# Optimization experiments

Measured on AMD Instinct MI355X. Metric: run time of the kernel, lower is better.

Reference implementation:

```python
import jax, jax.numpy as jnp
import numpy as np

HIDDEN = 1024
HEADS = 16
HEAD_DIM = HIDDEN // HEADS
ROPE_THETA = 10000.0
WINDOW = 128
NEG_INF = -1e9


def _rope_cos_sin(seq_len, head_dim, theta, dtype):
    # inv_freq: [dh/2]; emb = concat([freqs, freqs]) to match rotate-half convention
    inv_freq = 1.0 / (theta ** (jnp.arange(0, head_dim, 2, dtype=jnp.float32) / head_dim))
    pos = jnp.arange(seq_len, dtype=jnp.float32)
    freqs = jnp.einsum('s,d->sd', pos, inv_freq)          # [S, dh/2]
    emb = jnp.concatenate([freqs, freqs], axis=-1)        # [S, dh]
    return jnp.cos(emb).astype(dtype), jnp.sin(emb).astype(dtype)


def _apply_rope(x, cos, sin):
    # x: [B, S, H, dh]; cos/sin: [S, dh] broadcast over batch and heads
    x1, x2 = jnp.split(x, 2, axis=-1)
    half_rot = jnp.concatenate([-x2, x1], axis=-1)
    c = cos[None, :, None, :]
    s = sin[None, :, None, :]
    return x * c + half_rot * s


def setup_inputs() -> dict:
    key = jax.random.key(0)
    k1, k2, k3, k4, k5 = jax.random.split(key, 5)
    std = 0.02
    return {
        'hidden_states': jax.random.normal(k1, (2, 2048, HIDDEN), dtype=jnp.float32),
        'Wq': jax.random.normal(k2, (HIDDEN, HEADS, HEAD_DIM), dtype=jnp.float32) * std,
        'Wk': jax.random.normal(k3, (HIDDEN, HEADS, HEAD_DIM), dtype=jnp.float32) * std,
        'Wv': jax.random.normal(k4, (HIDDEN, HEADS, HEAD_DIM), dtype=jnp.float32) * std,
        'Wo': jax.random.normal(k5, (HEADS, HEAD_DIM, HIDDEN), dtype=jnp.float32) * std,
    }


def reference(hidden_states, Wq, Wk, Wv, Wo):
    B, S, D = hidden_states.shape
    x4 = hidden_states.reshape(B, S, HEADS, HEAD_DIM)
    cos, sin = _rope_cos_sin(S, HEAD_DIM, ROPE_THETA, hidden_states.dtype)
    # RoPE applied to raw hidden states (pre-projection), per original module
    q_in = _apply_rope(x4, cos, sin).reshape(B, S, D)
    k_in = q_in  # query and key get identical RoPE of the same tensor
    v_in = hidden_states

    q = jnp.einsum('bsd,dhk->bshk', q_in, Wq)  # [B,S,H,dh]
    k = jnp.einsum('bsd,dhk->bshk', k_in, Wk)
    v = jnp.einsum('bsd,dhk->bshk', v_in, Wv)

    scale = 1.0 / jnp.sqrt(jnp.asarray(HEAD_DIM, dtype=q.dtype))
    scores = jnp.einsum('bqhd,bkhd->bhqk', q, k) * scale  # [B,H,S,S]

    # sliding-window mask: |i - j| < WINDOW
    pos = jnp.arange(S)
    win = jnp.abs(pos[:, None] - pos[None, :]) < WINDOW   # [S,S] bool
    scores = jnp.where(win[None, None, :, :], scores, NEG_INF)

    probs = jax.nn.softmax(scores, axis=-1)
    out = jnp.einsum('bhqk,bkhd->bqhd', probs, v)          # [B,S,H,dh]
    return jnp.einsum('bqhd,hdo->bqo', out, Wo)            # [B,S,D]
```

## Files before the change

### kernel.cpp

```cpp
#include <hip/hip_runtime.h>
#include <hip/hip_bf16.h>
#include <cstdint>
#include <cmath>

typedef __bf16 bf16_t;
typedef __bf16 bf16x8 __attribute__((ext_vector_type(8)));
typedef __bf16 bf16x4 __attribute__((ext_vector_type(4)));
typedef float  f32x4  __attribute__((ext_vector_type(4)));
typedef float  f32x16 __attribute__((ext_vector_type(16)));

#define MFMA16(a, b, c) __builtin_amdgcn_mfma_f32_16x16x32_bf16(a, b, c, 0, 0, 0)
#define MFMA32(a, b, c) __builtin_amdgcn_mfma_f32_32x32x16_bf16(a, b, c, 0, 0, 0)

constexpr int   SS    = 2048;
constexpr int   DD    = 1024;
constexpr int   HH    = 16;
constexpr float SCALE = 0.125f;
constexpr float L2E   = 1.44269504088896f;

__device__ __forceinline__ bool detect_fp32(const uint16_t* w) {
    uint16_t v = w[threadIdx.x & 63];
    int e = (v >> 7) & 0xFF;
    unsigned long long m = __ballot(e >= 0x80);
    return __popcll(m) >= 4;
}

__device__ __forceinline__ float ldin(const void* p, size_t i, bool f32) {
    return f32 ? ((const float*)p)[i] : (float)((const bf16_t*)p)[i];
}

__device__ __forceinline__ void gload_lds16(const bf16_t* g, bf16_t* l) {
    __builtin_amdgcn_global_load_lds(
        (const __attribute__((address_space(1))) void*)(g),
        (__attribute__((address_space(3))) void*)(l), 16, 0, 0);
}

__global__ __launch_bounds__(256) void prep_kernel(
    const void* __restrict__ hidden, const void* __restrict__ Wq,
    const void* __restrict__ Wk, const void* __restrict__ Wv,
    const void* __restrict__ Wo,
    bf16_t* __restrict__ roped, bf16_t* __restrict__ hiddenb,
    bf16_t* __restrict__ WqT, bf16_t* __restrict__ WkT,
    bf16_t* __restrict__ WvT, bf16_t* __restrict__ WoT) {
    const bool f32 = detect_fp32((const uint16_t*)Wq);
    __shared__ bf16_t tile[32][33];
    if (blockIdx.x < 1024) {
        int gid = blockIdx.x * 256 + threadIdx.x;
        int ic = (gid & 3) * 8;
        int h  = (gid >> 2) & 15;
        int s  = (gid >> 6) & 2047;
        int b  = gid >> 17;
        size_t base = ((size_t)(b * SS + s)) * DD + h * 64 + ic;
        float x[8], y[8];
        if (f32) {
            const float* hp = (const float*)hidden;
            f32x4 x0 = *(const f32x4*)(hp + base);
            f32x4 x1 = *(const f32x4*)(hp + base + 4);
            f32x4 y0 = *(const f32x4*)(hp + base + 32);
            f32x4 y1 = *(const f32x4*)(hp + base + 36);
#pragma unroll
            for (int j = 0; j < 4; ++j) {
                x[j] = x0[j]; x[4 + j] = x1[j];
                y[j] = y0[j]; y[4 + j] = y1[j];
            }
        } else {
            const bf16_t* hp = (const bf16_t*)hidden;
            bf16x8 xv = *(const bf16x8*)(hp + base);
            bf16x8 yv = *(const bf16x8*)(hp + base + 32);
#pragma unroll
            for (int j = 0; j < 8; ++j) { x[j] = (float)xv[j]; y[j] = (float)yv[j]; }
        }
        bf16x8 ro, rh;
#pragma unroll
        for (int j = 0; j < 8; ++j) {
            int i = ic + j;
            float invf = exp2f(-(float)i * (13.287712379549449f / 32.0f));
            float sn, cs;
            __sincosf((float)s * invf, &sn, &cs);
            ro[j]  = (bf16_t)(x[j] * cs - y[j] * sn);
            rh[j]  = (bf16_t)(y[j] * cs + x[j] * sn);
        }
        *(bf16x8*)(roped + base)      = ro;
        *(bf16x8*)(roped + base + 32) = rh;
        if (f32) {
            bf16x8 hb0, hb1;
#pragma unroll
            for (int j = 0; j < 8; ++j) { hb0[j] = (bf16_t)x[j]; hb1[j] = (bf16_t)y[j]; }
            *(bf16x8*)(hiddenb + base)      = hb0;
            *(bf16x8*)(hiddenb + base + 32) = hb1;
        }
    } else {
        int w = blockIdx.x - 1024;
        int z = w >> 10;
        int yy = (w >> 5) & 31, xx = w & 31;
        const void* src = (z == 0) ? Wq : (z == 1) ? Wk : (z == 2) ? Wv : Wo;
        bf16_t*     dst = (z == 0) ? WqT : (z == 1) ? WkT : (z == 2) ? WvT : WoT;
        int tx = threadIdx.x & 31, ty = threadIdx.x >> 5;
        int x0 = xx * 32, y0 = yy * 32;
#pragma unroll
        for (int j = 0; j < 4; ++j)
            tile[ty + j * 8][tx] =
                (bf16_t)ldin(src, (size_t)(y0 + ty + j * 8) * DD + x0 + tx, f32);
        __syncthreads();
#pragma unroll
        for (int j = 0; j < 4; ++j)
            dst[(size_t)(x0 + ty + j * 8) * DD + y0 + tx] = tile[tx][ty + j * 8];
    }
}

__device__ __forceinline__ void stage_a128(const bf16_t* A, int m0, int k0,
                                           bf16_t* As, int tid) {
#pragma unroll
    for (int i = 0; i < 4; ++i) {
        int c = tid + i * 256;
        int r = c >> 3, g = (c & 7) ^ (r & 7);
        gload_lds16(A + (size_t)(m0 + r) * DD + k0 + g * 8, As + c * 8);
    }
}
__device__ __forceinline__ void stage_b64(const bf16_t* Bt, int n0, int k0,
                                          bf16_t* Bs, int tid) {
#pragma unroll
    for (int i = 0; i < 2; ++i) {
        int c = tid + i * 256;
        int r = c >> 3, g = (c & 7) ^ (r & 7);
        gload_lds16(Bt + (size_t)(n0 + r) * DD + k0 + g * 8, Bs + c * 8);
    }
}

__global__ __launch_bounds__(256, 4) void gemm_qkv_fused(
    const bf16_t* __restrict__ roped, const void* __restrict__ hidden_raw,
    const bf16_t* __restrict__ hiddenb, const uint16_t* __restrict__ wdet,
    const bf16_t* __restrict__ WqT, const bf16_t* __restrict__ WkT,
    const bf16_t* __restrict__ WvT,
    bf16_t* __restrict__ Qo, bf16_t* __restrict__ Ko, bf16_t* __restrict__ Vt) {
    __shared__ __align__(16) bf16_t As[128 * 64];
    __shared__ __align__(16) bf16_t B1[64 * 64];
    __shared__ __align__(16) bf16_t B2[64 * 64];
    const int tid = threadIdx.x, lane = tid & 63;
    const int l32 = lane & 31, kh = lane >> 5;
    const int wave = tid >> 6, wm = (wave >> 1) * 64, wn = (wave & 1) * 32;
    const int sw = l32 & 7;

    const int lin = blockIdx.x;
    const int z   = lin & 1;
    const int p   = lin >> 1;
    const int xcd = p & 7, rem = p >> 3;
    const int mb  = (xcd >> 1) * 8 + (rem >> 3);
    const int nb  = (xcd & 1) * 8 + (rem & 7);
    const int m0  = mb * 128, n0 = nb * 64;

    if (z == 0) {
        f32x16 accq[2], acck[2];
        accq[0] = (f32x16)0.0f; accq[1] = (f32x16)0.0f;
        acck[0] = (f32x16)0.0f; acck[1] = (f32x16)0.0f;
        for (int k0 = 0; k0 < DD; k0 += 64) {
            stage_a128(roped, m0, k0, As, tid);
            stage_b64(WqT, n0, k0, B1, tid);
            stage_b64(WkT, n0, k0, B2, tid);
            __syncthreads();
#pragma unroll
            for (int kk = 0; kk < 4; ++kk) {
                const int c8 = (kk * 2 + kh) ^ sw;
                bf16x8 a0 = *(const bf16x8*)(As + (wm      + l32) * 64 + c8 * 8);
                bf16x8 a1 = *(const bf16x8*)(As + (wm + 32 + l32) * 64 + c8 * 8);
                bf16x8 bq = *(const bf16x8*)(B1 + (wn + l32) * 64 + c8 * 8);
                bf16x8 bk = *(const bf16x8*)(B2 + (wn + l32) * 64 + c8 * 8);
                accq[0] = MFMA32(a0, bq, accq[0]);
                accq[1] = MFMA32(a1, bq, accq[1]);
                acck[0] = MFMA32(a0, bk, acck[0]);
                acck[1] = MFMA32(a1, bk, acck[1]);
            }
            __syncthreads();
        }
        const int d = wn + l32;
#pragma unroll
        for (int i = 0; i < 2; ++i) {
#pragma unroll
            for (int q4 = 0; q4 < 4; ++q4) {
                int row = m0 + wm + i * 32 + q4 * 8 + kh * 4;
                int bb = row >> 11, sl = row & 2047;
                size_t base = (((size_t)bb * HH + nb) * SS + sl) * 64 + d;
#pragma unroll
                for (int r = 0; r < 4; ++r) {
                    Qo[base + 64 * r] = (bf16_t)accq[i][q4 * 4 + r];
                    Ko[base + 64 * r] = (bf16_t)acck[i][q4 * 4 + r];
                }
            }
        }
    } else {
        const bool f32 = detect_fp32(wdet);
        const bf16_t* A = f32 ? hiddenb : (const bf16_t*)hidden_raw;
        f32x16 accv[2];
        accv[0] = (f32x16)0.0f; accv[1] = (f32x16)0.0f;
        for (int k0 = 0; k0 < DD; k0 += 64) {
            stage_a128(A, m0, k0, As, tid);
            stage_b64(WvT, n0, k0, B1, tid);
            __syncthreads();
#pragma unroll
            for (int kk = 0; kk < 4; ++kk) {
                const int c8 = (kk * 2 + kh) ^ sw;
                bf16x8 a0 = *(const bf16x8*)(As + (wm      + l32) * 64 + c8 * 8);
                bf16x8 a1 = *(const bf16x8*)(As + (wm + 32 + l32) * 64 + c8 * 8);
                bf16x8 bv = *(const bf16x8*)(B1 + (wn + l32) * 64 + c8 * 8);
                accv[0] = MFMA32(a0, bv, accv[0]);
                accv[1] = MFMA32(a1, bv, accv[1]);
            }
            __syncthreads();
        }
        const int d = wn + l32;
#pragma unroll
        for (int i = 0; i < 2; ++i) {
#pragma unroll
            for (int q4 = 0; q4 < 4; ++q4) {
                int row = m0 + wm + i * 32 + q4 * 8 + kh * 4;
                int bb = row >> 11, sl = row & 2047;
                bf16x4 v;
                v[0] = (bf16_t)accv[i][q4 * 4 + 0];
                v[1] = (bf16_t)accv[i][q4 * 4 + 1];
                v[2] = (bf16_t)accv[i][q4 * 4 + 2];
                v[3] = (bf16_t)accv[i][q4 * 4 + 3];
                *(bf16x4*)(Vt + (((size_t)bb * HH + nb) * 64 + d) * SS + sl) = v;
            }
        }
    }
}

__global__ __launch_bounds__(256) void attn_kernel(
    const bf16_t* __restrict__ Q, const bf16_t* __restrict__ Kk,
    const bf16_t* __restrict__ Vt, bf16_t* __restrict__ attn) {
    __shared__ __align__(16) bf16_t Ks[2][32 * 64];
    __shared__ __align__(16) bf16_t Vs[2][64 * 32];
    __shared__ __align__(16) bf16_t Pl[4][16 * 40];
    const int tid = threadIdx.x, wave = tid >> 6, lane = tid & 63;
    const int quad = lane >> 4, l16 = lane & 15;
    const int sw7 = l16 & 7, sw3 = l16 & 3;

    int lin = (blockIdx.x >> 3) + 128 * (blockIdx.x & 7);
    const int qb0 = (lin & 31) * 64;
    const int h   = (lin >> 5) & 15;
    const int b   = lin >> 9;
    const int qw  = qb0 + wave * 16;

    const size_t bh = (size_t)b * HH + h;
    const bf16_t* Qp = Q  + bh * SS * 64;
    const bf16_t* Kp = Kk + bh * SS * 64;
    const bf16_t* Vp = Vt + bh * 64 * SS;
    bf16_t* P = &Pl[wave][0];

    bf16x8 q0 = *(const bf16x8*)(Qp + (size_t)(qw + l16) * 64 + quad * 8);
    bf16x8 q1 = *(const bf16x8*)(Qp + (size_t)(qw + l16) * 64 + 32 + quad * 8);

    f32x4 Oacc[4];
#pragma unroll
    for (int t = 0; t < 4; ++t) Oacc[t] = (f32x4)0.0f;
    float lsum[4] = {0.f, 0.f, 0.f, 0.f};

    int lo = qb0 - 127; if (lo < 0) lo = 0; lo &= ~31;
    int hi = qb0 + 63 + 127; if (hi > SS - 1) hi = SS - 1;

    const int krow = tid >> 3, kcol = ((tid & 7) ^ (krow & 7)) * 8;
    const int vrow = tid >> 2, vcol = ((tid & 3) ^ (vrow & 3)) * 8;

    int parity = 0;
    for (int kt = lo; kt <= hi; kt += 32, parity ^= 1) {
        gload_lds16(Kp + (size_t)(kt + krow) * 64 + kcol, &Ks[parity][0] + tid * 8);
        gload_lds16(Vp + (size_t)vrow * SS + kt + vcol, &Vs[parity][0] + tid * 8);
        __syncthreads();

        const bf16_t* Kl = &Ks[parity][0];
        const bf16_t* Vl = &Vs[parity][0];
        bf16x8 k00 = *(const bf16x8*)(Kl + l16 * 64 + (quad ^ sw7) * 8);
        bf16x8 k01 = *(const bf16x8*)(Kl + l16 * 64 + ((quad + 4) ^ sw7) * 8);
        bf16x8 k10 = *(const bf16x8*)(Kl + (16 + l16) * 64 + (quad ^ sw7) * 8);
        bf16x8 k11 = *(const bf16x8*)(Kl + (16 + l16) * 64 + ((quad + 4) ^ sw7) * 8);
        bf16x8 vf[4];
#pragma unroll
        for (int t = 0; t < 4; ++t)
            vf[t] = *(const bf16x8*)(Vl + (t * 16 + l16) * 32 + (quad ^ sw3) * 8);

        f32x4 s0 = MFMA16(q0, k00, (f32x4)0.0f);  s0 = MFMA16(q1, k01, s0);
        f32x4 s1 = MFMA16(q0, k10, (f32x4)0.0f);  s1 = MFMA16(q1, k11, s1);

        const int kr0 = kt + l16, kr1 = kt + 16 + l16;
#pragma unroll
        for (int r = 0; r < 4; ++r) {
            int qa = qw + quad * 4 + r;
            int d0 = qa - kr0; if (d0 < 0) d0 = -d0;
            int d1 = qa - kr1; if (d1 < 0) d1 = -d1;
            float p0 = (d0 < 128) ? exp2f(s0[r] * (SCALE * L2E)) : 0.0f;
            float p1 = (d1 < 128) ? exp2f(s1[r] * (SCALE * L2E)) : 0.0f;
            lsum[r] += p0 + p1;
            P[(quad * 4 + r) * 40 + l16]      = (bf16_t)p0;
            P[(quad * 4 + r) * 40 + 16 + l16] = (bf16_t)p1;
        }
        __asm__ volatile("s_waitcnt lgkmcnt(0)" ::: "memory");
        bf16x8 pf = *(const bf16x8*)(P + l16 * 40 + quad * 8);
#pragma unroll
        for (int t = 0; t < 4; ++t)
            Oacc[t] = MFMA16(pf, vf[t], Oacc[t]);
    }

#pragma unroll
    for (int r = 0; r < 4; ++r) {
        float l = lsum[r];
        l += __shfl_xor(l, 1, 64);
        l += __shfl_xor(l, 2, 64);
        l += __shfl_xor(l, 4, 64);
        l += __shfl_xor(l, 8, 64);
        float inv = 1.0f / l;
        int sa = qw + quad * 4 + r;
        size_t base = (((size_t)b * SS + sa) * HH + h) * 64 + l16;
        attn[base]      = (bf16_t)(Oacc[0][r] * inv);
        attn[base + 16] = (bf16_t)(Oacc[1][r] * inv);
        attn[base + 32] = (bf16_t)(Oacc[2][r] * inv);
        attn[base + 48] = (bf16_t)(Oacc[3][r] * inv);
    }
}

__global__ __launch_bounds__(256, 4) void gemm_out_kernel(
    const bf16_t* __restrict__ A, const bf16_t* __restrict__ WoT,
    const uint16_t* __restrict__ wdet, void* __restrict__ out) {
    __shared__ __align__(16) bf16_t As[128 * 64];
    __shared__ __align__(16) bf16_t B1[64 * 64];
    const int tid = threadIdx.x, lane = tid & 63;
    const int l32 = lane & 31, kh = lane >> 5;
    const int wave = tid >> 6, wm = (wave >> 1) * 64, wn = (wave & 1) * 32;
    const int sw = l32 & 7;

    const int lin = blockIdx.x;
    const int xcd = lin & 7, s = lin >> 3;
    const int mb = (xcd >> 1) * 8 + (s >> 3);
    const int nb = (xcd & 1) * 8 + (s & 7);
    const int m0 = mb * 128, n0 = nb * 64;

    f32x16 acc[2];
    acc[0] = (f32x16)0.0f; acc[1] = (f32x16)0.0f;

    for (int k0 = 0; k0 < DD; k0 += 64) {
        stage_a128(A, m0, k0, As, tid);
        stage_b64(WoT, n0, k0, B1, tid);
        __syncthreads();
#pragma unroll
        for (int kk = 0; kk < 4; ++kk) {
            const int c8 = (kk * 2 + kh) ^ sw;
            bf16x8 a0 = *(const bf16x8*)(As + (wm      + l32) * 64 + c8 * 8);
            bf16x8 a1 = *(const bf16x8*)(As + (wm + 32 + l32) * 64 + c8 * 8);
            bf16x8 b0 = *(const bf16x8*)(B1 + (wn + l32) * 64 + c8 * 8);
            acc[0] = MFMA32(a0, b0, acc[0]);
            acc[1] = MFMA32(a1, b0, acc[1]);
        }
        __syncthreads();
    }

    const bool f32 = detect_fp32(wdet);
    const int n = n0 + wn + l32;
#pragma unroll
    for (int i = 0; i < 2; ++i) {
#pragma unroll
        for (int q4 = 0; q4 < 4; ++q4) {
            int row = m0 + wm + i * 32 + q4 * 8 + kh * 4;
#pragma unroll
            for (int r = 0; r < 4; ++r) {
                size_t idx = (size_t)(row + r) * DD + n;
                if (f32) ((float*)out)[idx] = acc[i][q4 * 4 + r];
                else     ((bf16_t*)out)[idx] = (bf16_t)acc[i][q4 * 4 + r];
            }
        }
    }
}

extern "C" void kernel_launch(void* const* d_in, const int* in_sizes, int n_in,
                              void* d_out, int out_size, void* d_ws, size_t ws_size,
                              hipStream_t stream) {
    const void* hidden = d_in[0];
    const void* Wq = d_in[1];
    const void* Wk = d_in[2];
    const void* Wv = d_in[3];
    const void* Wo = d_in[4];
    const uint16_t* wdet = (const uint16_t*)d_in[1];
    char* ws = (char*)d_ws;

    bf16_t* roped   = (bf16_t*)(ws);
    bf16_t* hiddenb = (bf16_t*)(ws + ( 8u << 20));
    bf16_t* WqT     = (bf16_t*)(ws + (16u << 20));
    bf16_t* WkT     = (bf16_t*)(ws + (18u << 20));
    bf16_t* WvT     = (bf16_t*)(ws + (20u << 20));
    bf16_t* WoT     = (bf16_t*)(ws + (22u << 20));
    bf16_t* Qb      = (bf16_t*)(ws + (24u << 20));
    bf16_t* Kb      = (bf16_t*)(ws + (32u << 20));
    bf16_t* Vt      = (bf16_t*)(ws + (40u << 20));
    bf16_t* attn    = roped;

    hipLaunchKernelGGL(prep_kernel, dim3(5120), dim3(256), 0, stream,
                       hidden, Wq, Wk, Wv, Wo, roped, hiddenb,
                       WqT, WkT, WvT, WoT);
    hipLaunchKernelGGL(gemm_qkv_fused, dim3(1024), dim3(256), 0, stream,
                       roped, hidden, hiddenb, wdet, WqT, WkT, WvT, Qb, Kb, Vt);
    hipLaunchKernelGGL(attn_kernel, dim3(1024), dim3(256), 0, stream,
                       Qb, Kb, Vt, attn);
    hipLaunchKernelGGL(gemm_out_kernel, dim3(512), dim3(256), 0, stream,
                       attn, WoT, wdet, d_out);
}
```

Baseline: 158.7 us.

## Fuse all four stages into one persistent kernel with grid barriers

Replaces the four separate launches (prep, QKV GEMM, attention, output GEMM) with one persistent 512-block kernel that loops over the former grids' tiles and separates stages with atomic-counter grid barriers. This is meant to remove kernel launch gaps and tail idle time between stages. It adds a memset launch, relies on all 512 blocks being co-resident (launch bounds set to 2 blocks/CU), and pays spin-wait barrier costs plus lower occupancy during the GEMM phases.

```diff
diff --git a/kernel.cpp b/kernel.cpp
--- a/kernel.cpp
+++ b/kernel.cpp
@@ -35,335 +35,361 @@
         (__attribute__((address_space(3))) void*)(l), 16, 0, 0);
 }
 
-__global__ __launch_bounds__(256) void prep_kernel(
+__device__ __forceinline__ void stage_a128(const bf16_t* A, int m0, int k0,
+                                           bf16_t* As, int tid) {
+#pragma unroll
+    for (int i = 0; i < 4; ++i) {
+        int c = tid + i * 256;
+        int r = c >> 3, g = (c & 7) ^ (r & 7);
+        gload_lds16(A + (size_t)(m0 + r) * DD + k0 + g * 8, As + c * 8);
+    }
+}
+__device__ __forceinline__ void stage_b64(const bf16_t* Bt, int n0, int k0,
+                                          bf16_t* Bs, int tid) {
+#pragma unroll
+    for (int i = 0; i < 2; ++i) {
+        int c = tid + i * 256;
+        int r = c >> 3, g = (c & 7) ^ (r & 7);
+        gload_lds16(Bt + (size_t)(n0 + r) * DD + k0 + g * 8, Bs + c * 8);
+    }
+}
+
+__device__ __forceinline__ void grid_bar(unsigned* w) {
+    __syncthreads();
+    if (threadIdx.x == 0) {
+        __threadfence();
+        if (atomicAdd(w, 1u) == 511u) {
+            atomicExch(w + 1, 1u);
+        } else {
+            while (atomicOr(w + 1, 0u) == 0u) __builtin_amdgcn_s_sleep(8);
+        }
+        __threadfence();
+    }
+    __syncthreads();
+}
+
+__global__ __launch_bounds__(256, 2) void mega_kernel(
     const void* __restrict__ hidden, const void* __restrict__ Wq,
     const void* __restrict__ Wk, const void* __restrict__ Wv,
     const void* __restrict__ Wo,
     bf16_t* __restrict__ roped, bf16_t* __restrict__ hiddenb,
     bf16_t* __restrict__ WqT, bf16_t* __restrict__ WkT,
-    bf16_t* __restrict__ WvT, bf16_t* __restrict__ WoT) {
+    bf16_t* __restrict__ WvT, bf16_t* __restrict__ WoT,
+    bf16_t* __restrict__ Qb, bf16_t* __restrict__ Kb,
+    bf16_t* __restrict__ Vt, bf16_t* __restrict__ attnb,
+    void* __restrict__ out, unsigned* __restrict__ bars) {
+    __shared__ __align__(16) char smem[32768];
+    const int tid  = threadIdx.x, lane = tid & 63;
     const bool f32 = detect_fp32((const uint16_t*)Wq);
-    __shared__ bf16_t tile[32][33];
-    if (blockIdx.x < 1024) {
-        int gid = blockIdx.x * 256 + threadIdx.x;
-        int ic = (gid & 3) * 8;
-        int h  = (gid >> 2) & 15;
-        int s  = (gid >> 6) & 2047;
-        int b  = gid >> 17;
-        size_t base = ((size_t)(b * SS + s)) * DD + h * 64 + ic;
-        float x[8], y[8];
-        if (f32) {
-            const float* hp = (const float*)hidden;
-            f32x4 x0 = *(const f32x4*)(hp + base);
-            f32x4 x1 = *(const f32x4*)(hp + base + 4);
-            f32x4 y0 = *(const f32x4*)(hp + base + 32);
-            f32x4 y1 = *(const f32x4*)(hp + base + 36);
-#pragma unroll
-            for (int j = 0; j < 4; ++j) {
-                x[j] = x0[j]; x[4 + j] = x1[j];
-                y[j] = y0[j]; y[4 + j] = y1[j];
-            }
-        } else {
-            const bf16_t* hp = (const bf16_t*)hidden;
-            bf16x8 xv = *(const bf16x8*)(hp + base);
-            bf16x8 yv = *(const bf16x8*)(hp + base + 32);
-#pragma unroll
-            for (int j = 0; j < 8; ++j) { x[j] = (float)xv[j]; y[j] = (float)yv[j]; }
-        }
-        bf16x8 ro, rh;
-#pragma unroll
-        for (int j = 0; j < 8; ++j) {
-            int i = ic + j;
-            float invf = exp2f(-(float)i * (13.287712379549449f / 32.0f));
-            float sn, cs;
-            __sincosf((float)s * invf, &sn, &cs);
-            ro[j]  = (bf16_t)(x[j] * cs - y[j] * sn);
-            rh[j]  = (bf16_t)(y[j] * cs + x[j] * sn);
-        }
-        *(bf16x8*)(roped + base)      = ro;
-        *(bf16x8*)(roped + base + 32) = rh;
-        if (f32) {
-            bf16x8 hb0, hb1;
-#pragma unroll
-            for (int j = 0; j < 8; ++j) { hb0[j] = (bf16_t)x[j]; hb1[j] = (bf16_t)y[j]; }
-            *(bf16x8*)(hiddenb + base)      = hb0;
-            *(bf16x8*)(hiddenb + base + 32) = hb1;
-        }
-    } else {
-        int w = blockIdx.x - 1024;
-        int z = w >> 10;
-        int yy = (w >> 5) & 31, xx = w & 31;
-        const void* src = (z == 0) ? Wq : (z == 1) ? Wk : (z == 2) ? Wv : Wo;
-        bf16_t*     dst = (z == 0) ? WqT : (z == 1) ? WkT : (z == 2) ? WvT : WoT;
-        int tx = threadIdx.x & 31, ty = threadIdx.x >> 5;
-        int x0 = xx * 32, y0 = yy * 32;
-#pragma unroll
-        for (int j = 0; j < 4; ++j)
-            tile[ty + j * 8][tx] =
-                (bf16_t)ldin(src, (size_t)(y0 + ty + j * 8) * DD + x0 + tx, f32);
-        __syncthreads();
-#pragma unroll
-        for (int j = 0; j < 4; ++j)
-            dst[(size_t)(x0 + ty + j * 8) * DD + y0 + tx] = tile[tx][ty + j * 8];
-    }
-}
-
-__device__ __forceinline__ void stage_a128(const bf16_t* A, int m0, int k0,
-                                           bf16_t* As, int tid) {
-#pragma unroll
-    for (int i = 0; i < 4; ++i) {
-        int c = tid + i * 256;
-        int r = c >> 3, g = (c & 7) ^ (r & 7);
-        gload_lds16(A + (size_t)(m0 + r) * DD + k0 + g * 8, As + c * 8);
-    }
-}
-__device__ __forceinline__ void stage_b64(const bf16_t* Bt, int n0, int k0,
-                                          bf16_t* Bs, int tid) {
-#pragma unroll
-    for (int i = 0; i < 2; ++i) {
-        int c = tid + i * 256;
-        int r = c >> 3, g = (c & 7) ^ (r & 7);
-        gload_lds16(Bt + (size_t)(n0 + r) * DD + k0 + g * 8, Bs + c * 8);
-    }
-}
-
-__global__ __launch_bounds__(256, 4) void gemm_qkv_fused(
-    const bf16_t* __restrict__ roped, const void* __restrict__ hidden_raw,
-    const bf16_t* __restrict__ hiddenb, const uint16_t* __restrict__ wdet,
-    const bf16_t* __restrict__ WqT, const bf16_t* __restrict__ WkT,
-    const bf16_t* __restrict__ WvT,
-    bf16_t* __restrict__ Qo, bf16_t* __restrict__ Ko, bf16_t* __restrict__ Vt) {
-    __shared__ __align__(16) bf16_t As[128 * 64];
-    __shared__ __align__(16) bf16_t B1[64 * 64];
-    __shared__ __align__(16) bf16_t B2[64 * 64];
-    const int tid = threadIdx.x, lane = tid & 63;
-    const int l32 = lane & 31, kh = lane >> 5;
-    const int wave = tid >> 6, wm = (wave >> 1) * 64, wn = (wave & 1) * 32;
-    const int sw = l32 & 7;
-
-    const int lin = blockIdx.x;
-    const int z   = lin & 1;
-    const int p   = lin >> 1;
-    const int xcd = p & 7, rem = p >> 3;
-    const int mb  = (xcd >> 1) * 8 + (rem >> 3);
-    const int nb  = (xcd & 1) * 8 + (rem & 7);
-    const int m0  = mb * 128, n0 = nb * 64;
-
-    if (z == 0) {
-        f32x16 accq[2], acck[2];
-        accq[0] = (f32x16)0.0f; accq[1] = (f32x16)0.0f;
-        acck[0] = (f32x16)0.0f; acck[1] = (f32x16)0.0f;
+
+    {
+        bf16_t (*tile)[33] = reinterpret_cast<bf16_t(*)[33]>(smem);
+        for (int vb = blockIdx.x; vb < 5120; vb += 512) {
+            if (vb < 1024) {
+                int gid = vb * 256 + tid;
+                int ic = (gid & 3) * 8;
+                int h  = (gid >> 2) & 15;
+                int s  = (gid >> 6) & 2047;
+                int b  = gid >> 17;
+                size_t base = ((size_t)(b * SS + s)) * DD + h * 64 + ic;
+                float x[8], y[8];
+                if (f32) {
+                    const float* hp = (const float*)hidden;
+                    f32x4 x0 = *(const f32x4*)(hp + base);
+                    f32x4 x1 = *(const f32x4*)(hp + base + 4);
+                    f32x4 y0 = *(const f32x4*)(hp + base + 32);
+                    f32x4 y1 = *(const f32x4*)(hp + base + 36);
+#pragma unroll
+                    for (int j = 0; j < 4; ++j) {
+                        x[j] = x0[j]; x[4 + j] = x1[j];
+                        y[j] = y0[j]; y[4 + j] = y1[j];
+                    }
+                } else {
+                    const bf16_t* hp = (const bf16_t*)hidden;
+                    bf16x8 xv = *(const bf16x8*)(hp + base);
+                    bf16x8 yv = *(const bf16x8*)(hp + base + 32);
+#pragma unroll
+                    for (int j = 0; j < 8; ++j) { x[j] = (float)xv[j]; y[j] = (float)yv[j]; }
+                }
+                bf16x8 ro, rh;
+#pragma unroll
+                for (int j = 0; j < 8; ++j) {
+                    int i = ic + j;
+                    float invf = exp2f(-(float)i * (13.287712379549449f / 32.0f));
+                    float sn, cs;
+                    __sincosf((float)s * invf, &sn, &cs);
+                    ro[j] = (bf16_t)(x[j] * cs - y[j] * sn);
+                    rh[j] = (bf16_t)(y[j] * cs + x[j] * sn);
+                }
+                *(bf16x8*)(roped + base)      = ro;
+                *(bf16x8*)(roped + base + 32) = rh;
+                if (f32) {
+                    bf16x8 hb0, hb1;
+#pragma unroll
+                    for (int j = 0; j < 8; ++j) { hb0[j] = (bf16_t)x[j]; hb1[j] = (bf16_t)y[j]; }
+                    *(bf16x8*)(hiddenb + base)      = hb0;
+                    *(bf16x8*)(hiddenb + base + 32) = hb1;
+                }
+            } else {
+                int w = vb - 1024;
+                int z = w >> 10;
+                int yy = (w >> 5) & 31, xx = w & 31;
+                const void* src = (z == 0) ? Wq : (z == 1) ? Wk : (z == 2) ? Wv : Wo;
+                bf16_t*     dst = (z == 0) ? WqT : (z == 1) ? WkT : (z == 2) ? WvT : WoT;
+                int tx = tid & 31, ty = tid >> 5;
+                int x0 = xx * 32, y0 = yy * 32;
+#pragma unroll
+                for (int j = 0; j < 4; ++j)
+                    tile[ty + j * 8][tx] =
+                        (bf16_t)ldin(src, (size_t)(y0 + ty + j * 8) * DD + x0 + tx, f32);
+                __syncthreads();
+#pragma unroll
+                for (int j = 0; j < 4; ++j)
+                    dst[(size_t)(x0 + ty + j * 8) * DD + y0 + tx] = tile[tx][ty + j * 8];
+                __syncthreads();
+            }
+        }
+    }
+    grid_bar(bars + 0);
+
+    {
+        bf16_t* As = (bf16_t*)smem;
+        bf16_t* B1 = (bf16_t*)(smem + 16384);
+        bf16_t* B2 = (bf16_t*)(smem + 24576);
+        const int l32 = lane & 31, kh = lane >> 5;
+        const int wave = tid >> 6, wm = (wave >> 1) * 64, wn = (wave & 1) * 32;
+        const int sw = l32 & 7;
+#pragma unroll 1
+        for (int rpt = 0; rpt < 2; ++rpt) {
+            const int lin = (rpt == 0) ? (int)blockIdx.x : 1023 - (int)blockIdx.x;
+            const int z   = lin & 1;
+            const int p   = lin >> 1;
+            const int xcd = p & 7, rem = p >> 3;
+            const int mb  = (xcd >> 1) * 8 + (rem >> 3);
+            const int nb  = (xcd & 1) * 8 + (rem & 7);
+            const int m0  = mb * 128, n0 = nb * 64;
+
+            if (z == 0) {
+                f32x16 accq[2], acck[2];
+                accq[0] = (f32x16)0.0f; accq[1] = (f32x16)0.0f;
+                acck[0] = (f32x16)0.0f; acck[1] = (f32x16)0.0f;
+                for (int k0 = 0; k0 < DD; k0 += 64) {
+                    stage_a128(roped, m0, k0, As, tid);
+                    stage_b64(WqT, n0, k0, B1, tid);
+                    stage_b64(WkT, n0, k0, B2, tid);
+                    __syncthreads();
+#pragma unroll
+                    for (int kk = 0; kk < 4; ++kk) {
+                        const int c8 = (kk * 2 + kh) ^ sw;
+                        bf16x8 a0 = *(const bf16x8*)(As + (wm      + l32) * 64 + c8 * 8);
+                        bf16x8 a1 = *(const bf16x8*)(As + (wm + 32 + l32) * 64 + c8 * 8);
+                        bf16x8 bq = *(const bf16x8*)(B1 + (wn + l32) * 64 + c8 * 8);
+                        bf16x8 bk = *(const bf16x8*)(B2 + (wn + l32) * 64 + c8 * 8);
+                        accq[0] = MFMA32(a0, bq, accq[0]);
+                        accq[1] = MFMA32(a1, bq, accq[1]);
+                        acck[0] = MFMA32(a0, bk, acck[0]);
+                        acck[1] = MFMA32(a1, bk, acck[1]);
+                    }
+                    __syncthreads();
+                }
+                const int d = wn + l32;
+#pragma unroll
+                for (int i = 0; i < 2; ++i) {
+#pragma unroll
+                    for (int q4 = 0; q4 < 4; ++q4) {
+                        int row = m0 + wm + i * 32 + q4 * 8 + kh * 4;
+                        int bb = row >> 11, sl = row & 2047;
+                        size_t base = (((size_t)bb * HH + nb) * SS + sl) * 64 + d;
+#pragma unroll
+                        for (int r = 0; r < 4; ++r) {
+                            Qb[base + 64 * r] = (bf16_t)accq[i][q4 * 4 + r];
+                            Kb[base + 64 * r] = (bf16_t)acck[i][q4 * 4 + r];
+                        }
+                    }
+                }
+            } else {
+                const bf16_t* A = f32 ? hiddenb : (const bf16_t*)hidden;
+                f32x16 accv[2];
+                accv[0] = (f32x16)0.0f; accv[1] = (f32x16)0.0f;
+                for (int k0 = 0; k0 < DD; k0 += 64) {
+                    stage_a128(A, m0, k0, As, tid);
+                    stage_b64(WvT, n0, k0, B1, tid);
+                    __syncthreads();
+#pragma unroll
+                    for (int kk = 0; kk < 4; ++kk) {
+                        const int c8 = (kk * 2 + kh) ^ sw;
+                        bf16x8 a0 = *(const bf16x8*)(As + (wm      + l32) * 64 + c8 * 8);
+                        bf16x8 a1 = *(const bf16x8*)(As + (wm + 32 + l32) * 64 + c8 * 8);
+                        bf16x8 bv = *(const bf16x8*)(B1 + (wn + l32) * 64 + c8 * 8);
+                        accv[0] = MFMA32(a0, bv, accv[0]);
+                        accv[1] = MFMA32(a1, bv, accv[1]);
+                    }
+                    __syncthreads();
+                }
+                const int d = wn + l32;
+#pragma unroll
+                for (int i = 0; i < 2; ++i) {
+#pragma unroll
+                    for (int q4 = 0; q4 < 4; ++q4) {
+                        int row = m0 + wm + i * 32 + q4 * 8 + kh * 4;
+                        int bb = row >> 11, sl = row & 2047;
+                        bf16x4 v;
+                        v[0] = (bf16_t)accv[i][q4 * 4 + 0];
+                        v[1] = (bf16_t)accv[i][q4 * 4 + 1];
+                        v[2] = (bf16_t)accv[i][q4 * 4 + 2];
+                        v[3] = (bf16_t)accv[i][q4 * 4 + 3];
+                        *(bf16x4*)(Vt + (((size_t)bb * HH + nb) * 64 + d) * SS + sl) = v;
+                    }
+                }
+            }
+            __syncthreads();
+        }
+    }
+    grid_bar(bars + 2);
+
+    {
+        bf16_t* KsB = (bf16_t*)smem;
+        bf16_t* VsB = (bf16_t*)(smem + 8192);
+        bf16_t* PlB = (bf16_t*)(smem + 16384);
+        const int wave = tid >> 6;
+        const int quad = lane >> 4, l16 = lane & 15;
+        const int sw7 = l16 & 7, sw3 = l16 & 3;
+        bf16_t* P = PlB + wave * 640;
+
+#pragma unroll 1
+        for (int rpt = 0; rpt < 2; ++rpt) {
+            const int vt = (int)blockIdx.x + rpt * 512;
+            int lin = (vt >> 3) + 128 * (vt & 7);
+            const int qb0 = (lin & 31) * 64;
+            const int h   = (lin >> 5) & 15;
+            const int b   = lin >> 9;
+            const int qw  = qb0 + wave * 16;
+
+            const size_t bh = (size_t)b * HH + h;
+            const bf16_t* Qp = Qb + bh * SS * 64;
+            const bf16_t* Kp = Kb + bh * SS * 64;
+            const bf16_t* Vp = Vt + bh * 64 * SS;
+
+            bf16x8 q0 = *(const bf16x8*)(Qp + (size_t)(qw + l16) * 64 + quad * 8);
+            bf16x8 q1 = *(const bf16x8*)(Qp + (size_t)(qw + l16) * 64 + 32 + quad * 8);
+
+            f32x4 Oacc[4];
+#pragma unroll
+            for (int t = 0; t < 4; ++t) Oacc[t] = (f32x4)0.0f;
+            float lsum[4] = {0.f, 0.f, 0.f, 0.f};
+
+            int lo = qb0 - 127; if (lo < 0) lo = 0; lo &= ~31;
+            int hi = qb0 + 63 + 127; if (hi > SS - 1) hi = SS - 1;
+
+            const int krow = tid >> 3, kcol = ((tid & 7) ^ (krow & 7)) * 8;
+            const int vrow = tid >> 2, vcol = ((tid & 3) ^ (vrow & 3)) * 8;
+
+            int parity = 0;
+            for (int kt = lo; kt <= hi; kt += 32, parity ^= 1) {
+                gload_lds16(Kp + (size_t)(kt + krow) * 64 + kcol,
+                            KsB + parity * 2048 + tid * 8);
+                gload_lds16(Vp + (size_t)vrow * SS + kt + vcol,
+                            VsB + parity * 2048 + tid * 8);
+                __syncthreads();
+
+                const bf16_t* Kl = KsB + parity * 2048;
+                const bf16_t* Vl = VsB + parity * 2048;
+                bf16x8 k00 = *(const bf16x8*)(Kl + l16 * 64 + (quad ^ sw7) * 8);
+                bf16x8 k01 = *(const bf16x8*)(Kl + l16 * 64 + ((quad + 4) ^ sw7) * 8);
+                bf16x8 k10 = *(const bf16x8*)(Kl + (16 + l16) * 64 + (quad ^ sw7) * 8);
+                bf16x8 k11 = *(const bf16x8*)(Kl + (16 + l16) * 64 + ((quad + 4) ^ sw7) * 8);
+                bf16x8 vf[4];
+#pragma unroll
+                for (int t = 0; t < 4; ++t)
+                    vf[t] = *(const bf16x8*)(Vl + (t * 16 + l16) * 32 + (quad ^ sw3) * 8);
+
+                f32x4 s0 = MFMA16(q0, k00, (f32x4)0.0f);  s0 = MFMA16(q1, k01, s0);
+                f32x4 s1 = MFMA16(q0, k10, (f32x4)0.0f);  s1 = MFMA16(q1, k11, s1);
+
+                const int kr0 = kt + l16, kr1 = kt + 16 + l16;
+#pragma unroll
+                for (int r = 0; r < 4; ++r) {
+                    int qa = qw + quad * 4 + r;
+                    int d0 = qa - kr0; if (d0 < 0) d0 = -d0;
+                    int d1 = qa - kr1; if (d1 < 0) d1 = -d1;
+                    float p0 = (d0 < 128) ? exp2f(s0[r] * (SCALE * L2E)) : 0.0f;
+                    float p1 = (d1 < 128) ? exp2f(s1[r] * (SCALE * L2E)) : 0.0f;
+                    lsum[r] += p0 + p1;
+                    P[(quad * 4 + r) * 40 + l16]      = (bf16_t)p0;
+                    P[(quad * 4 + r) * 40 + 16 + l16] = (bf16_t)p1;
+                }
+                __asm__ volatile("s_waitcnt lgkmcnt(0)" ::: "memory");
+                __builtin_amdgcn_sched_barrier(0);
+                bf16x8 pf = *(const bf16x8*)(P + l16 * 40 + quad * 8);
+#pragma unroll
+                for (int t = 0; t < 4; ++t)
+                    Oacc[t] = MFMA16(pf, vf[t], Oacc[t]);
+            }
+            __syncthreads();
+
+#pragma unroll
+            for (int r = 0; r < 4; ++r) {
+                float l = lsum[r];
+                l += __shfl_xor(l, 1, 64);
+                l += __shfl_xor(l, 2, 64);
+                l += __shfl_xor(l, 4, 64);
+                l += __shfl_xor(l, 8, 64);
+                float inv = 1.0f / l;
+                int sa = qw + quad * 4 + r;
+                size_t base = (((size_t)b * SS + sa) * HH + h) * 64 + l16;
+                attnb[base]      = (bf16_t)(Oacc[0][r] * inv);
+                attnb[base + 16] = (bf16_t)(Oacc[1][r] * inv);
+                attnb[base + 32] = (bf16_t)(Oacc[2][r] * inv);
+                attnb[base + 48] = (bf16_t)(Oacc[3][r] * inv);
+            }
+        }
+    }
+    grid_bar(bars + 4);
+
+    {
+        bf16_t* As = (bf16_t*)smem;
+        bf16_t* B1 = (bf16_t*)(smem + 16384);
+        const int l32 = lane & 31, kh = lane >> 5;
+        const int wave = tid >> 6, wm = (wave >> 1) * 64, wn = (wave & 1) * 32;
+        const int sw = l32 & 7;
+
+        const int lin = blockIdx.x;
+        const int xcd = lin & 7, s = lin >> 3;
+        const int mb = (xcd >> 1) * 8 + (s >> 3);
+        const int nb = (xcd & 1) * 8 + (s & 7);
+        const int m0 = mb * 128, n0 = nb * 64;
+
+        f32x16 acc[2];
+        acc[0] = (f32x16)0.0f; acc[1] = (f32x16)0.0f;
+
         for (int k0 = 0; k0 < DD; k0 += 64) {
-            stage_a128(roped, m0, k0, As, tid);
-            stage_b64(WqT, n0, k0, B1, tid);
-            stage_b64(WkT, n0, k0, B2, tid);
+            stage_a128(attnb, m0, k0, As, tid);
+            stage_b64(WoT, n0, k0, B1, tid);
             __syncthreads();
 #pragma unroll
             for (int kk = 0; kk < 4; ++kk) {
                 const int c8 = (kk * 2 + kh) ^ sw;
                 bf16x8 a0 = *(const bf16x8*)(As + (wm      + l32) * 64 + c8 * 8);
                 bf16x8 a1 = *(const bf16x8*)(As + (wm + 32 + l32) * 64 + c8 * 8);
-                bf16x8 bq = *(const bf16x8*)(B1 + (wn + l32) * 64 + c8 * 8);
-                bf16x8 bk = *(const bf16x8*)(B2 + (wn + l32) * 64 + c8 * 8);
-                accq[0] = MFMA32(a0, bq, accq[0]);
-                accq[1] = MFMA32(a1, bq, accq[1]);
-                acck[0] = MFMA32(a0, bk, acck[0]);
-                acck[1] = MFMA32(a1, bk, acck[1]);
+                bf16x8 b0 = *(const bf16x8*)(B1 + (wn + l32) * 64 + c8 * 8);
+                acc[0] = MFMA32(a0, b0, acc[0]);
+                acc[1] = MFMA32(a1, b0, acc[1]);
             }
             __syncthreads();
         }
-        const int d = wn + l32;
+
+        const int n = n0 + wn + l32;
 #pragma unroll
         for (int i = 0; i < 2; ++i) {
 #pragma unroll
             for (int q4 = 0; q4 < 4; ++q4) {
                 int row = m0 + wm + i * 32 + q4 * 8 + kh * 4;
-                int bb = row >> 11, sl = row & 2047;
-                size_t base = (((size_t)bb * HH + nb) * SS + sl) * 64 + d;
 #pragma unroll
                 for (int r = 0; r < 4; ++r) {
-                    Qo[base + 64 * r] = (bf16_t)accq[i][q4 * 4 + r];
-                    Ko[base + 64 * r] = (bf16_t)acck[i][q4 * 4 + r];
-                }
-            }
-        }
-    } else {
-        const bool f32 = detect_fp32(wdet);
-        const bf16_t* A = f32 ? hiddenb : (const bf16_t*)hidden_raw;
-        f32x16 accv[2];
-        accv[0] = (f32x16)0.0f; accv[1] = (f32x16)0.0f;
-        for (int k0 = 0; k0 < DD; k0 += 64) {
-            stage_a128(A, m0, k0, As, tid);
-            stage_b64(WvT, n0, k0, B1, tid);
-            __syncthreads();
-#pragma unroll
-            for (int kk = 0; kk < 4; ++kk) {
-                const int c8 = (kk * 2 + kh) ^ sw;
-                bf16x8 a0 = *(const bf16x8*)(As + (wm      + l32) * 64 + c8 * 8);
-                bf16x8 a1 = *(const bf16x8*)(As + (wm + 32 + l32) * 64 + c8 * 8);
-                bf16x8 bv = *(const bf16x8*)(B1 + (wn + l32) * 64 + c8 * 8);
-                accv[0] = MFMA32(a0, bv, accv[0]);
-                accv[1] = MFMA32(a1, bv, accv[1]);
-            }
-            __syncthreads();
-        }
-        const int d = wn + l32;
-#pragma unroll
-        for (int i = 0; i < 2; ++i) {
-#pragma unroll
-            for (int q4 = 0; q4 < 4; ++q4) {
-                int row = m0 + wm + i * 32 + q4 * 8 + kh * 4;
-                int bb = row >> 11, sl = row & 2047;
-                bf16x4 v;
-                v[0] = (bf16_t)accv[i][q4 * 4 + 0];
-                v[1] = (bf16_t)accv[i][q4 * 4 + 1];
-                v[2] = (bf16_t)accv[i][q4 * 4 + 2];
-                v[3] = (bf16_t)accv[i][q4 * 4 + 3];
-                *(bf16x4*)(Vt + (((size_t)bb * HH + nb) * 64 + d) * SS + sl) = v;
-            }
-        }
-    }
-}
-
-__global__ __launch_bounds__(256) void attn_kernel(
-    const bf16_t* __restrict__ Q, const bf16_t* __restrict__ Kk,
-    const bf16_t* __restrict__ Vt, bf16_t* __restrict__ attn) {
-    __shared__ __align__(16) bf16_t Ks[2][32 * 64];
-    __shared__ __align__(16) bf16_t Vs[2][64 * 32];
-    __shared__ __align__(16) bf16_t Pl[4][16 * 40];
-    const int tid = threadIdx.x, wave = tid >> 6, lane = tid & 63;
-    const int quad = lane >> 4, l16 = lane & 15;
-    const int sw7 = l16 & 7, sw3 = l16 & 3;
-
-    int lin = (blockIdx.x >> 3) + 128 * (blockIdx.x & 7);
-    const int qb0 = (lin & 31) * 64;
-    const int h   = (lin >> 5) & 15;
-    const int b   = lin >> 9;
-    const int qw  = qb0 + wave * 16;
-
-    const size_t bh = (size_t)b * HH + h;
-    const bf16_t* Qp = Q  + bh * SS * 64;
-    const bf16_t* Kp = Kk + bh * SS * 64;
-    const bf16_t* Vp = Vt + bh * 64 * SS;
-    bf16_t* P = &Pl[wave][0];
-
-    bf16x8 q0 = *(const bf16x8*)(Qp + (size_t)(qw + l16) * 64 + quad * 8);
-    bf16x8 q1 = *(const bf16x8*)(Qp + (size_t)(qw + l16) * 64 + 32 + quad * 8);
-
-    f32x4 Oacc[4];
-#pragma unroll
-    for (int t = 0; t < 4; ++t) Oacc[t] = (f32x4)0.0f;
-    float lsum[4] = {0.f, 0.f, 0.f, 0.f};
-
-    int lo = qb0 - 127; if (lo < 0) lo = 0; lo &= ~31;
-    int hi = qb0 + 63 + 127; if (hi > SS - 1) hi = SS - 1;
-
-    const int krow = tid >> 3, kcol = ((tid & 7) ^ (krow & 7)) * 8;
-    const int vrow = tid >> 2, vcol = ((tid & 3) ^ (vrow & 3)) * 8;
-
-    int parity = 0;
-    for (int kt = lo; kt <= hi; kt += 32, parity ^= 1) {
-        gload_lds16(Kp + (size_t)(kt + krow) * 64 + kcol, &Ks[parity][0] + tid * 8);
-        gload_lds16(Vp + (size_t)vrow * SS + kt + vcol, &Vs[parity][0] + tid * 8);
-        __syncthreads();
-
-        const bf16_t* Kl = &Ks[parity][0];
-        const bf16_t* Vl = &Vs[parity][0];
-        bf16x8 k00 = *(const bf16x8*)(Kl + l16 * 64 + (quad ^ sw7) * 8);
-        bf16x8 k01 = *(const bf16x8*)(Kl + l16 * 64 + ((quad + 4) ^ sw7) * 8);
-        bf16x8 k10 = *(const bf16x8*)(Kl + (16 + l16) * 64 + (quad ^ sw7) * 8);
-        bf16x8 k11 = *(const bf16x8*)(Kl + (16 + l16) * 64 + ((quad + 4) ^ sw7) * 8);
-        bf16x8 vf[4];
-#pragma unroll
-        for (int t = 0; t < 4; ++t)
-            vf[t] = *(const bf16x8*)(Vl + (t * 16 + l16) * 32 + (quad ^ sw3) * 8);
-
-        f32x4 s0 = MFMA16(q0, k00, (f32x4)0.0f);  s0 = MFMA16(q1, k01, s0);
-        f32x4 s1 = MFMA16(q0, k10, (f32x4)0.0f);  s1 = MFMA16(q1, k11, s1);
-
-        const int kr0 = kt + l16, kr1 = kt + 16 + l16;
-#pragma unroll
-        for (int r = 0; r < 4; ++r) {
-            int qa = qw + quad * 4 + r;
-            int d0 = qa - kr0; if (d0 < 0) d0 = -d0;
-            int d1 = qa - kr1; if (d1 < 0) d1 = -d1;
-            float p0 = (d0 < 128) ? exp2f(s0[r] * (SCALE * L2E)) : 0.0f;
-            float p1 = (d1 < 128) ? exp2f(s1[r] * (SCALE * L2E)) : 0.0f;
-            lsum[r] += p0 + p1;
-            P[(quad * 4 + r) * 40 + l16]      = (bf16_t)p0;
-            P[(quad * 4 + r) * 40 + 16 + l16] = (bf16_t)p1;
-        }
-        __asm__ volatile("s_waitcnt lgkmcnt(0)" ::: "memory");
-        bf16x8 pf = *(const bf16x8*)(P + l16 * 40 + quad * 8);
-#pragma unroll
-        for (int t = 0; t < 4; ++t)
-            Oacc[t] = MFMA16(pf, vf[t], Oacc[t]);
-    }
-
-#pragma unroll
-    for (int r = 0; r < 4; ++r) {
-        float l = lsum[r];
-        l += __shfl_xor(l, 1, 64);
-        l += __shfl_xor(l, 2, 64);
-        l += __shfl_xor(l, 4, 64);
-        l += __shfl_xor(l, 8, 64);
-        float inv = 1.0f / l;
-        int sa = qw + quad * 4 + r;
-        size_t base = (((size_t)b * SS + sa) * HH + h) * 64 + l16;
-        attn[base]      = (bf16_t)(Oacc[0][r] * inv);
-        attn[base + 16] = (bf16_t)(Oacc[1][r] * inv);
-        attn[base + 32] = (bf16_t)(Oacc[2][r] * inv);
-        attn[base + 48] = (bf16_t)(Oacc[3][r] * inv);
-    }
-}
-
-__global__ __launch_bounds__(256, 4) void gemm_out_kernel(
-    const bf16_t* __restrict__ A, const bf16_t* __restrict__ WoT,
-    const uint16_t* __restrict__ wdet, void* __restrict__ out) {
-    __shared__ __align__(16) bf16_t As[128 * 64];
-    __shared__ __align__(16) bf16_t B1[64 * 64];
-    const int tid = threadIdx.x, lane = tid & 63;
-    const int l32 = lane & 31, kh = lane >> 5;
-    const int wave = tid >> 6, wm = (wave >> 1) * 64, wn = (wave & 1) * 32;
-    const int sw = l32 & 7;
-
-    const int lin = blockIdx.x;
-    const int xcd = lin & 7, s = lin >> 3;
-    const int mb = (xcd >> 1) * 8 + (s >> 3);
-    const int nb = (xcd & 1) * 8 + (s & 7);
-    const int m0 = mb * 128, n0 = nb * 64;
-
-    f32x16 acc[2];
-    acc[0] = (f32x16)0.0f; acc[1] = (f32x16)0.0f;
-
-    for (int k0 = 0; k0 < DD; k0 += 64) {
-        stage_a128(A, m0, k0, As, tid);
-        stage_b64(WoT, n0, k0, B1, tid);
-        __syncthreads();
-#pragma unroll
-        for (int kk = 0; kk < 4; ++kk) {
-            const int c8 = (kk * 2 + kh) ^ sw;
-            bf16x8 a0 = *(const bf16x8*)(As + (wm      + l32) * 64 + c8 * 8);
-            bf16x8 a1 = *(const bf16x8*)(As + (wm + 32 + l32) * 64 + c8 * 8);
-            bf16x8 b0 = *(const bf16x8*)(B1 + (wn + l32) * 64 + c8 * 8);
-            acc[0] = MFMA32(a0, b0, acc[0]);
-            acc[1] = MFMA32(a1, b0, acc[1]);
-        }
-        __syncthreads();
-    }
-
-    const bool f32 = detect_fp32(wdet);
-    const int n = n0 + wn + l32;
-#pragma unroll
-    for (int i = 0; i < 2; ++i) {
-#pragma unroll
-        for (int q4 = 0; q4 < 4; ++q4) {
-            int row = m0 + wm + i * 32 + q4 * 8 + kh * 4;
-#pragma unroll
-            for (int r = 0; r < 4; ++r) {
-                size_t idx = (size_t)(row + r) * DD + n;
-                if (f32) ((float*)out)[idx] = acc[i][q4 * 4 + r];
-                else     ((bf16_t*)out)[idx] = (bf16_t)acc[i][q4 * 4 + r];
+                    size_t idx = (size_t)(row + r) * DD + n;
+                    if (f32) ((float*)out)[idx] = acc[i][q4 * 4 + r];
+                    else     ((bf16_t*)out)[idx] = (bf16_t)acc[i][q4 * 4 + r];
+                }
             }
         }
     }
@@ -377,7 +403,6 @@
     const void* Wk = d_in[2];
     const void* Wv = d_in[3];
     const void* Wo = d_in[4];
-    const uint16_t* wdet = (const uint16_t*)d_in[1];
     char* ws = (char*)d_ws;
 
     bf16_t* roped   = (bf16_t*)(ws);
@@ -389,15 +414,12 @@
     bf16_t* Qb      = (bf16_t*)(ws + (24u << 20));
     bf16_t* Kb      = (bf16_t*)(ws + (32u << 20));
     bf16_t* Vt      = (bf16_t*)(ws + (40u << 20));
-    bf16_t* attn    = roped;
-
-    hipLaunchKernelGGL(prep_kernel, dim3(5120), dim3(256), 0, stream,
+    bf16_t* attnb   = (bf16_t*)(ws + (48u << 20));
+    unsigned* bars  = (unsigned*)(ws + (60u << 20));
+
+    hipMemsetAsync(bars, 0, 256, stream);
+
+    hipLaunchKernelGGL(mega_kernel, dim3(512), dim3(256), 0, stream,
                        hidden, Wq, Wk, Wv, Wo, roped, hiddenb,
-                       WqT, WkT, WvT, WoT);
-    hipLaunchKernelGGL(gemm_qkv_fused, dim3(1024), dim3(256), 0, stream,
-                       roped, hidden, hiddenb, wdet, WqT, WkT, WvT, Qb, Kb, Vt);
-    hipLaunchKernelGGL(attn_kernel, dim3(1024), dim3(256), 0, stream,
-                       Qb, Kb, Vt, attn);
-    hipLaunchKernelGGL(gemm_out_kernel, dim3(512), dim3(256), 0, stream,
-                       attn, WoT, wdet, d_out);
-}
+                       WqT, WkT, WvT, WoT, Qb, Kb, Vt, attnb, d_out, bars);
+}
```

New measurement: 326.1 us. 2.06x slower.
